# Kernel optimization log

Hardware: AMD Instinct MI355X
Metric: run time of the kernel (lower is better)

## Reference

```python
import jax, jax.numpy as jnp
import numpy as np

NB, DM, DIN, DS, DTR, K = 4, 64, 128, 16, 4, 4
C, COUT, H, W, BATCH, NH = 256, 256, 32, 32, 4, 8


def layernorm(x, w, b, eps=1e-5):
    mu = x.mean(-1, keepdims=True)
    var = ((x - mu) ** 2).mean(-1, keepdims=True)
    return (x - mu) * jax.lax.rsqrt(var + eps) * w + b


def ln_hw(x, eps=1e-5):
    # F.layer_norm(x, [H, W]) -> normalize over last two dims, no affine
    mu = x.mean((-2, -1), keepdims=True)
    var = ((x - mu) ** 2).mean((-2, -1), keepdims=True)
    return (x - mu) * jax.lax.rsqrt(var + eps)


def conv1d(x, w, b, groups=1, pad=1):
    # x: (B, Cin, L), w: (Cout, Cin//groups, k)
    y = jax.lax.conv_general_dilated(x, w, (1,), [(pad, pad)],
                                     dimension_numbers=('NCH', 'OIH', 'NCH'),
                                     feature_group_count=groups)
    return y + b[None, :, None]


def selective_scan(u, dt, Bm, Cm, A, Dp):
    # u, dt: (B,L,din); Bm, Cm: (B,L,ds); A: (din,ds); Dp: (din,)
    dA = jnp.exp(dt[..., None] * A)                     # (B,L,din,ds)
    dBu = (dt * u)[..., None] * Bm[:, :, None, :]       # (B,L,din,ds)

    def step(h, inp):
        dA_t, dBu_t, C_t = inp
        h = dA_t * h + dBu_t
        return h, jnp.einsum('bds,bs->bd', h, C_t)

    h0 = jnp.zeros((u.shape[0], DIN, DS), u.dtype)
    _, ys = jax.lax.scan(step, h0, (dA.transpose(1, 0, 2, 3), dBu.transpose(1, 0, 2, 3), Cm.transpose(1, 0, 2)))
    return ys.transpose(1, 0, 2) + u * Dp


def mamba(xs, inw, convw, convb, xpw, dtw, dtb, alog, dp, outw):
    # xs: (B,L,DM) one branch of Mamba(d_model=DM, d_state=DS, d_conv=K, expand=2)
    xz = xs @ inw.T                                     # (B,L,2*DIN)
    u, z = jnp.split(xz, 2, axis=-1)
    # causal depthwise conv1d (torch pads K-1 and truncates to L == left pad K-1)
    uc = jax.lax.conv_general_dilated(u.transpose(0, 2, 1), convw[:, None, :], (1,), [(K - 1, 0)],
                                      dimension_numbers=('NCH', 'OIH', 'NCH'),
                                      feature_group_count=DIN) + convb[None, :, None]
    u = jax.nn.silu(uc.transpose(0, 2, 1))              # (B,L,DIN)
    xdbc = u @ xpw.T                                    # (B,L,DTR+2*DS)
    dt = jax.nn.softplus(xdbc[..., :DTR] @ dtw.T + dtb)
    Bm, Cm = xdbc[..., DTR:DTR + DS], xdbc[..., DTR + DS:]
    y = selective_scan(u, dt, Bm, Cm, -jnp.exp(alog), dp)
    return (y * jax.nn.silu(z)) @ outw.T


mamba_v = jax.vmap(mamba)  # over branch axis 0 of inputs and all params


def mha(x, inw, inb, outw, outb):
    B, N, Cc = x.shape
    hd = Cc // NH
    qkv = x @ inw.T + inb
    q, k, v = jnp.split(qkv, 3, axis=-1)
    q = q.reshape(B, N, NH, hd).transpose(0, 2, 1, 3)
    k = k.reshape(B, N, NH, hd).transpose(0, 2, 1, 3)
    v = v.reshape(B, N, NH, hd).transpose(0, 2, 1, 3)
    att = jax.nn.softmax((q @ k.transpose(0, 1, 3, 2)) * (1.0 / (hd ** 0.5)), axis=-1)
    o = (att @ v).transpose(0, 2, 1, 3).reshape(B, N, Cc)
    return o @ outw.T + outb


def reference(x, norm_w, norm_b, skip_scale, m_inw, m_convw, m_convb, m_xpw, m_dtw, m_dtb, m_alog, m_d, m_outw, qdw_w, qdw_b, qpw_w, qpw_b, rdw_w, rdw_b, rpw_w, rpw_b, fdw_w, fdw_b, fpw_w, fpw_b, lc_w, lc_b, attn_inw, attn_inb, attn_outw, attn_outb, lgn_w, lgn_b, fc_w, fc_b, dwc_w, dwc_b, proj_w, proj_b):
    B, Cc, Hh, Ww = x.shape
    N = Hh * Ww
    xs = x.reshape(B, Cc, N).transpose(0, 2, 1)         # (B,N,C)
    xn = layernorm(xs, norm_w, norm_b)
    # channel-chunk into NB branches: (NB,B,N,DM)
    xc = xn.reshape(B, N, NB, DM).transpose(2, 0, 1, 3)
    xm = mamba_v(xc, m_inw, m_convw, m_convb, m_xpw, m_dtw, m_dtb, m_alog, m_d, m_outw) + skip_scale * xc
    x_concat = xm.transpose(1, 2, 0, 3).reshape(B, N, Cc)
    # branch gating: depthwise grouped conv (C->NB) then pointwise (NB->NB)
    Q = conv1d(conv1d(x_concat.transpose(0, 2, 1), qdw_w, qdw_b, groups=NB, pad=1), qpw_w, qpw_b, groups=1, pad=0)
    g = jax.nn.sigmoid(Q)                               # (B,NB,N)
    xg = (g.transpose(1, 0, 2)[..., None] * xm).transpose(1, 2, 0, 3).reshape(B, N, Cc)
    xgt = xg.transpose(0, 2, 1)                          # (B,C,N)
    R = conv1d(conv1d(xgt, rdw_w, rdw_b, groups=Cc, pad=1), rpw_w, rpw_b, groups=1, pad=0) + xgt
    cat = jnp.concatenate([xs, R.transpose(0, 2, 1)], axis=-1).transpose(0, 2, 1)  # (B,2C,N)
    xm2 = conv1d(conv1d(cat, fdw_w, fdw_b, groups=2 * Cc, pad=1), fpw_w, fpw_b, groups=1, pad=0) + cat[:, :Cc, :]
    xm2 = xm2.transpose(0, 2, 1)                         # (B,N,C)
    # local-global feature mixing
    x_local = conv1d(xm2.transpose(0, 2, 1), lc_w, lc_b, groups=Cc, pad=1).transpose(0, 2, 1)
    x_global = mha(xm2, attn_inw, attn_inb, attn_outw, attn_outb)
    x_out = jnp.concatenate([x_local, x_global], axis=-1) @ fc_w.T + fc_b
    x_out = jax.nn.gelu(layernorm(x_out, lgn_w, lgn_b), approximate=False)
    # DepthwiseConvolution: layer_norm over [H,W] (no affine) then depthwise conv2d
    xi = x_out.transpose(0, 2, 1).reshape(B, Cc, Hh, Ww)
    xi = ln_hw(xi)
    xi = jax.lax.conv_general_dilated(xi, dwc_w, (1, 1), [(1, 1), (1, 1)],
                                      dimension_numbers=('NCHW', 'OIHW', 'NCHW'),
                                      feature_group_count=Cc) + dwc_b[None, :, None, None]
    x_mixed = xi.reshape(B, Cc, N).transpose(0, 2, 1)
    x_mixed = layernorm(x_mixed, norm_w, norm_b)        # self.norm reused
    x_mixed = x_mixed @ proj_w.T + proj_b
    return x_mixed.transpose(0, 2, 1).reshape(B, COUT, Hh, Ww)


def setup_inputs() -> dict:
    key = jax.random.key(0)
    ks = iter(jax.random.split(key, 64))

    def rn(shape, s=0.02):
        return jax.random.normal(next(ks), shape, jnp.float32) * s

    return dict(
        x=jax.random.normal(next(ks), (BATCH, C, H, W), jnp.float32),
        norm_w=jnp.ones((C,), jnp.float32), norm_b=jnp.zeros((C,), jnp.float32),
        skip_scale=jnp.ones((1,), jnp.float32),
        m_inw=rn((NB, 2 * DIN, DM)), m_convw=rn((NB, DIN, K), 0.2), m_convb=jnp.zeros((NB, DIN), jnp.float32),
        m_xpw=rn((NB, DTR + 2 * DS, DIN)), m_dtw=rn((NB, DIN, DTR), 0.2), m_dtb=rn((NB, DIN), 0.5),
        m_alog=jnp.tile(jnp.log(jnp.arange(1, DS + 1, dtype=jnp.float32)), (NB, DIN, 1)),
        m_d=jnp.ones((NB, DIN), jnp.float32), m_outw=rn((NB, DM, DIN)),
        qdw_w=rn((NB, C // NB, 3), 0.1), qdw_b=jnp.zeros((NB,), jnp.float32),
        qpw_w=rn((NB, NB, 1), 0.3), qpw_b=jnp.zeros((NB,), jnp.float32),
        rdw_w=rn((C, 1, 3), 0.2), rdw_b=jnp.zeros((C,), jnp.float32),
        rpw_w=rn((C, C, 1)), rpw_b=jnp.zeros((C,), jnp.float32),
        fdw_w=rn((2 * C, 1, 3), 0.2), fdw_b=jnp.zeros((2 * C,), jnp.float32),
        fpw_w=rn((C, 2 * C, 1)), fpw_b=jnp.zeros((C,), jnp.float32),
        lc_w=rn((C, 1, 3), 0.2), lc_b=jnp.zeros((C,), jnp.float32),
        attn_inw=rn((3 * C, C)), attn_inb=jnp.zeros((3 * C,), jnp.float32),
        attn_outw=rn((C, C)), attn_outb=jnp.zeros((C,), jnp.float32),
        lgn_w=jnp.ones((C,), jnp.float32), lgn_b=jnp.zeros((C,), jnp.float32),
        fc_w=rn((C, 2 * C)), fc_b=jnp.zeros((C,), jnp.float32),
        dwc_w=rn((C, 1, 3, 3), 0.2), dwc_b=jnp.zeros((C,), jnp.float32),
        proj_w=rn((COUT, C)), proj_b=jnp.zeros((COUT,), jnp.float32),
    )
```

## Files before the change

### kernel.cpp

```cpp
#include <hip/hip_runtime.h>
#include <math.h>


namespace {
constexpr int NB_ = 4, DM_ = 64, DIN_ = 128, DS_ = 16, DTR_ = 4;
constexpr int C_ = 256, N_ = 1024, B_ = 4, HD_ = 32;
constexpr int NCH = 16, LCH = 64;
constexpr int NSTATE = 16 * 128 * 16;
}

typedef __attribute__((ext_vector_type(8))) short bf16x8;
typedef __attribute__((ext_vector_type(4))) float f32x4;
typedef __attribute__((ext_vector_type(8))) unsigned short ushort8v;
typedef __attribute__((ext_vector_type(4))) unsigned short ushort4v;

__device__ __forceinline__ unsigned short f2b(float f) {
  unsigned int u = __float_as_uint(f);
  unsigned int r = u + 0x7FFFu + ((u >> 16) & 1u);
  return (unsigned short)(r >> 16);
}

__device__ __forceinline__ float2 blockReduce2(float a, float b, float* red) {
#pragma unroll
  for (int m = 1; m < 64; m <<= 1) {
    a += __shfl_xor(a, m, 64);
    b += __shfl_xor(b, m, 64);
  }
  int w = threadIdx.x >> 6;
  if ((threadIdx.x & 63) == 0) { red[2 * w] = a; red[2 * w + 1] = b; }
  __syncthreads();
  float ra = red[0] + red[2] + red[4] + red[6];
  float rb = red[1] + red[3] + red[5] + red[7];
  return make_float2(ra, rb);
}

__device__ __forceinline__ float siluf(float x) { return x / (1.f + expf(-x)); }
__device__ __forceinline__ float sigmf(float x) { return 1.f / (1.f + expf(-x)); }
__device__ __forceinline__ float softplusf(float x) {
  return fmaxf(x, 0.f) + log1pf(expf(-fabsf(x)));
}

__global__ __launch_bounds__(256) void k_ln_t2(const float* __restrict__ in,
                                               const float* __restrict__ w,
                                               const float* __restrict__ bias,
                                               float* __restrict__ out_ln) {
  __shared__ float tile[256][17];
  __shared__ float redp[16][16][2];
  __shared__ float stats[16][2];
  int bx = blockIdx.x;
  int b = bx >> 6, n0 = (bx & 63) * 16;
  int c = threadIdx.x;
  {
    const float* p = in + ((long)(b * C_ + c)) * N_ + n0;
#pragma unroll
    for (int j = 0; j < 16; ++j) tile[c][j] = p[j];
  }
  __syncthreads();
  {
    int n = c & 15, g = c >> 4;
    float a = 0.f, q = 0.f;
#pragma unroll
    for (int i = 0; i < 16; ++i) {
      float v = tile[g * 16 + i][n];
      a += v; q += v * v;
    }
    redp[g][n][0] = a; redp[g][n][1] = q;
  }
  __syncthreads();
  if (c < 16) {
    float a = 0.f, q = 0.f;
#pragma unroll
    for (int g2 = 0; g2 < 16; ++g2) { a += redp[g2][c][0]; q += redp[g2][c][1]; }
    float mu = a * (1.f / C_);
    float rs = rsqrtf(q * (1.f / C_) - mu * mu + 1e-5f);
    stats[c][0] = mu; stats[c][1] = rs;
  }
  __syncthreads();
  float wv = w[c], bv = bias[c];
#pragma unroll
  for (int j = 0; j < 16; ++j) {
    float v = tile[c][j];
    long o = ((long)(b * N_ + n0 + j)) * C_ + c;
    out_ln[o] = (v - stats[j][0]) * stats[j][1] * wv + bv;
  }
}

__global__ __launch_bounds__(256) void k_inproj_conv(const float* __restrict__ xn,
                                                     const float* __restrict__ inw,
                                                     const float* __restrict__ cw,
                                                     const float* __restrict__ cb,
                                                     float* __restrict__ U,
                                                     float* __restrict__ Z) {
  __shared__ unsigned short xa[64][72];
  __shared__ unsigned short wb[64][72];
  __shared__ float ut[67][65];
  int r0 = blockIdx.x * 64;
  int nb = blockIdx.y >> 2, q = blockIdx.y & 3, c0 = q * 64;
  int t = threadIdx.x;
  int wv = t >> 6, lane = t & 63, g = lane >> 4, ql = lane & 15;
  const f32x4 zf = {0.f, 0.f, 0.f, 0.f};
  f32x4 acc[4] = {zf, zf, zf, zf};
  int rr = t >> 2, kq = (t & 3) * 16;
  {
    const float* xsrc = xn + (long)(r0 + rr) * C_ + nb * 64 + kq;
#pragma unroll
    for (int j = 0; j < 4; ++j) {
      float4 v = *(const float4*)(xsrc + 4 * j);
      ushort4v u = {f2b(v.x), f2b(v.y), f2b(v.z), f2b(v.w)};
      *(ushort4v*)&xa[rr][kq + 4 * j] = u;
    }
    const float* wsrc = inw + ((long)nb * 256 + c0 + rr) * 64 + kq;
#pragma unroll
    for (int j = 0; j < 4; ++j) {
      float4 v = *(const float4*)(wsrc + 4 * j);
      ushort4v u = {f2b(v.x), f2b(v.y), f2b(v.z), f2b(v.w)};
      *(ushort4v*)&wb[rr][kq + 4 * j] = u;
    }
  }
  __syncthreads();
#pragma unroll
  for (int ks = 0; ks < 2; ++ks) {
    bf16x8 a = *(const bf16x8*)&xa[wv * 16 + ql][ks * 32 + g * 8];
#pragma unroll
    for (int ct = 0; ct < 4; ++ct) {
      bf16x8 b = *(const bf16x8*)&wb[ct * 16 + ql][ks * 32 + g * 8];
      acc[ct] = __builtin_amdgcn_mfma_f32_16x16x32_bf16(a, b, acc[ct], 0, 0, 0);
    }
  }
  if (q < 2) {
#pragma unroll
    for (int ct = 0; ct < 4; ++ct)
#pragma unroll
      for (int reg = 0; reg < 4; ++reg)
        ut[3 + wv * 16 + g * 4 + reg][ct * 16 + ql] = acc[ct][reg];
    if (t < 192) {
      int hr = t >> 6, lc = t & 63;
      float hv = 0.f;
      if ((r0 & 1023) != 0) {
        const float* xrow = xn + (long)(r0 - 3 + hr) * C_ + nb * 64;
        const float* wrow = inw + ((long)nb * 256 + c0 + lc) * 64;
#pragma unroll 8
        for (int k = 0; k < 64; ++k) hv += xrow[k] * wrow[k];
      }
      ut[hr][lc] = hv;
    }
    __syncthreads();
#pragma unroll
    for (int ct = 0; ct < 4; ++ct) {
      int lc = ct * 16 + ql;
      int d = c0 + lc;
      const float* cwp = cw + (nb * DIN_ + d) * 4;
      float w0 = cwp[0], w1 = cwp[1], w2 = cwp[2], w3 = cwp[3];
      float bv = cb[nb * DIN_ + d];
#pragma unroll
      for (int reg = 0; reg < 4; ++reg) {
        int lr = wv * 16 + g * 4 + reg;
        float a = bv + w3 * ut[3 + lr][lc] + w2 * ut[2 + lr][lc] +
                  w1 * ut[1 + lr][lc] + w0 * ut[lr][lc];
        long row = (long)nb * 4096 + r0 + lr;
        U[row * DIN_ + d] = siluf(a);
      }
    }
  } else {
#pragma unroll
    for (int ct = 0; ct < 4; ++ct) {
      int col = c0 - 128 + ct * 16 + ql;
#pragma unroll
      for (int reg = 0; reg < 4; ++reg) {
        long row = (long)nb * 4096 + r0 + wv * 16 + g * 4 + reg;
        Z[row * DIN_ + col] = acc[ct][reg];
      }
    }
  }
}

__global__ __launch_bounds__(256) void k_xdbc_mfma(const float* __restrict__ U,
                                                   const float* __restrict__ xpw,
                                                   const float* __restrict__ dtw,
                                                   const float* __restrict__ dtb,
                                                   float* __restrict__ DT,
                                                   float* __restrict__ BMb,
                                                   float* __restrict__ CMb) {
  __shared__ unsigned short xa[64][72];
  __shared__ unsigned short wb[48][72];
  __shared__ float xd_s[64][40];
  __shared__ float dtw_s[128][4];
  __shared__ float dtb_s[128];
  int t = threadIdx.x;
  long row0 = (long)blockIdx.x * 64;
  int nb = blockIdx.x >> 6;
  for (int i = t; i < 512; i += 256) dtw_s[i >> 2][i & 3] = dtw[nb * 512 + i];
  if (t < 128) dtb_s[t] = dtb[nb * DIN_ + t];
  int wv = t >> 6, lane = t & 63, g = lane >> 4, ql = lane & 15;
  const f32x4 zf = {0.f, 0.f, 0.f, 0.f};
  f32x4 acc[3] = {zf, zf, zf};
  int rr = t >> 2, kq = (t & 3) * 16;
  for (int k0 = 0; k0 < 128; k0 += 64) {
    __syncthreads();
    const float* xsrc = U + (row0 + rr) * DIN_ + k0 + kq;
#pragma unroll
    for (int j = 0; j < 4; ++j) {
      float4 v = *(const float4*)(xsrc + 4 * j);
      ushort4v u = {f2b(v.x), f2b(v.y), f2b(v.z), f2b(v.w)};
      *(ushort4v*)&xa[rr][kq + 4 * j] = u;
    }
    if (rr < 48) {
      if (rr < 36) {
        const float* wsrc = xpw + (long)nb * 36 * 128 + rr * 128 + k0 + kq;
#pragma unroll
        for (int j = 0; j < 4; ++j) {
          float4 v = *(const float4*)(wsrc + 4 * j);
          ushort4v u = {f2b(v.x), f2b(v.y), f2b(v.z), f2b(v.w)};
          *(ushort4v*)&wb[rr][kq + 4 * j] = u;
        }
      } else {
        ushort4v z = {0, 0, 0, 0};
#pragma unroll
        for (int j = 0; j < 4; ++j) *(ushort4v*)&wb[rr][kq + 4 * j] = z;
      }
    }
    __syncthreads();
#pragma unroll
    for (int ks = 0; ks < 2; ++ks) {
      bf16x8 a = *(const bf16x8*)&xa[wv * 16 + ql][ks * 32 + g * 8];
#pragma unroll
      for (int ct = 0; ct < 3; ++ct) {
        bf16x8 b = *(const bf16x8*)&wb[ct * 16 + ql][ks * 32 + g * 8];
        acc[ct] = __builtin_amdgcn_mfma_f32_16x16x32_bf16(a, b, acc[ct], 0, 0, 0);
      }
    }
  }
#pragma unroll
  for (int ct = 0; ct < 3; ++ct) {
    int col = ct * 16 + ql;
    if (col < 36) {
#pragma unroll
      for (int reg = 0; reg < 4; ++reg)
        xd_s[wv * 16 + g * 4 + reg][col] = acc[ct][reg];
    }
  }
  __syncthreads();
  {
    int r = t >> 2, sq = (t & 3) * 4;
    float4 bm4 = make_float4(xd_s[r][4 + sq], xd_s[r][5 + sq],
                             xd_s[r][6 + sq], xd_s[r][7 + sq]);
    *(float4*)&BMb[(row0 + r) * DS_ + sq] = bm4;
    float4 cm4 = make_float4(xd_s[r][20 + sq], xd_s[r][21 + sq],
                             xd_s[r][22 + sq], xd_s[r][23 + sq]);
    *(float4*)&CMb[(row0 + r) * DS_ + sq] = cm4;
  }
  {
    int r = t >> 2, dg = t & 3;
    float x0 = xd_s[r][0], x1 = xd_s[r][1], x2 = xd_s[r][2], x3 = xd_s[r][3];
    float* dst = DT + (row0 + r) * DIN_ + dg * 32;
#pragma unroll
    for (int j = 0; j < 8; ++j) {
      float o[4];
#pragma unroll
      for (int e = 0; e < 4; ++e) {
        int d = dg * 32 + j * 4 + e;
        float a = dtb_s[d] + x0 * dtw_s[d][0] + x1 * dtw_s[d][1] +
                  x2 * dtw_s[d][2] + x3 * dtw_s[d][3];
        o[e] = softplusf(a);
      }
      *(float4*)(dst + j * 4) = make_float4(o[0], o[1], o[2], o[3]);
    }
  }
}

__global__ __launch_bounds__(256) void k_scanA(const float* __restrict__ DT,
                                               const float* __restrict__ U,
                                               const float* __restrict__ BMb,
                                               const float* __restrict__ alog,
                                               float* __restrict__ Aprod,
                                               float* __restrict__ Hend) {
  __shared__ float dt_s[64][64];
  __shared__ float u_s[64][64];
  __shared__ float bm_s[64][16];
  int bx = blockIdx.x;
  int chunk = bx >> 5, rem = bx & 31, nbb = rem >> 1, dh = rem & 1;
  int nb = nbb >> 2;
  int t = threadIdx.x;
  int dl = t >> 2, sg = t & 3;
  int d = dh * 64 + dl;
  long base = (long)nbb * N_ + chunk * LCH;
#pragma unroll
  for (int j = 0; j < 4; ++j) {
    int f = t + 256 * j;
    int tt = f >> 4, dq = (f & 15) * 4;
    long src = (base + tt) * DIN_ + dh * 64 + dq;
    *(float4*)&dt_s[tt][dq] = *(const float4*)&DT[src];
    *(float4*)&u_s[tt][dq]  = *(const float4*)&U[src];
  }
  {
    int tt = t >> 2, sq = (t & 3) * 4;
    *(float4*)&bm_s[tt][sq] = *(const float4*)&BMb[(base + tt) * DS_ + sq];
  }
  float A[4];
#pragma unroll
  for (int i = 0; i < 4; ++i)
    A[i] = -expf(alog[(nb * DIN_ + d) * DS_ + sg * 4 + i]);
  __syncthreads();
  float h[4] = {0.f, 0.f, 0.f, 0.f};
  float ap[4] = {1.f, 1.f, 1.f, 1.f};
  for (int tt = 0; tt < LCH; ++tt) {
    float dtv = dt_s[tt][dl];
    float uv  = u_s[tt][dl];
    float cc = dtv * uv;
    float4 bm4 = *(const float4*)&bm_s[tt][sg * 4];
    float bmv[4] = {bm4.x, bm4.y, bm4.z, bm4.w};
#pragma unroll
    for (int i = 0; i < 4; ++i) {
      float dA = __expf(dtv * A[i]);
      h[i] = dA * h[i] + cc * bmv[i];
      ap[i] *= dA;
    }
  }
  long st = (long)chunk * NSTATE + ((nbb << 7) + d) * 16 + sg * 4;
  *(float4*)&Aprod[st] = make_float4(ap[0], ap[1], ap[2], ap[3]);
  *(float4*)&Hend[st]  = make_float4(h[0], h[1], h[2], h[3]);
}

__global__ __launch_bounds__(256) void k_scanC(float* __restrict__ DT,
                                               const float* __restrict__ U,
                                               const float* __restrict__ BMb,
                                               const float* __restrict__ CMb,
                                               const float* __restrict__ alog,
                                               const float* __restrict__ Dp,
                                               const float* __restrict__ Aprod,
                                               const float* __restrict__ Hend) {
  __shared__ float dt_s[64][64];
  __shared__ float u_s[64][64];
  __shared__ float bm_s[64][16];
  __shared__ float cm_s[64][16];
  int bx = blockIdx.x;
  int chunk = bx >> 5, rem = bx & 31, nbb = rem >> 1, dh = rem & 1;
  int nb = nbb >> 2;
  int t = threadIdx.x;
  int dl = t >> 2, sg = t & 3;
  int d = dh * 64 + dl;
  long base = (long)nbb * N_ + chunk * LCH;
#pragma unroll
  for (int j = 0; j < 4; ++j) {
    int f = t + 256 * j;
    int tt = f >> 4, dq = (f & 15) * 4;
    long src = (base + tt) * DIN_ + dh * 64 + dq;
    *(float4*)&dt_s[tt][dq] = *(const float4*)&DT[src];
    *(float4*)&u_s[tt][dq]  = *(const float4*)&U[src];
  }
  {
    int tt = t >> 2, sq = (t & 3) * 4;
    *(float4*)&bm_s[tt][sq] = *(const float4*)&BMb[(base + tt) * DS_ + sq];
    *(float4*)&cm_s[tt][sq] = *(const float4*)&CMb[(base + tt) * DS_ + sq];
  }
  float A[4];
#pragma unroll
  for (int i = 0; i < 4; ++i)
    A[i] = -expf(alog[(nb * DIN_ + d) * DS_ + sg * 4 + i]);
  float Dv = Dp[nb * DIN_ + d];
  float h[4] = {0.f, 0.f, 0.f, 0.f};
  {
    long state4 = ((nbb << 7) + d) * 16 + sg * 4;
    for (int c = 0; c < chunk; ++c) {
      float4 a4 = *(const float4*)&Aprod[(long)c * NSTATE + state4];
      float4 e4 = *(const float4*)&Hend[(long)c * NSTATE + state4];
      h[0] = e4.x + a4.x * h[0];
      h[1] = e4.y + a4.y * h[1];
      h[2] = e4.z + a4.z * h[2];
      h[3] = e4.w + a4.w * h[3];
    }
  }
  __syncthreads();
  for (int tt = 0; tt < LCH; ++tt) {
    float dtv = dt_s[tt][dl];
    float uv  = u_s[tt][dl];
    float cc = dtv * uv;
    float4 bm4 = *(const float4*)&bm_s[tt][sg * 4];
    float4 cm4 = *(const float4*)&cm_s[tt][sg * 4];
    float bmv[4] = {bm4.x, bm4.y, bm4.z, bm4.w};
    float cmv[4] = {cm4.x, cm4.y, cm4.z, cm4.w};
    float p = 0.f;
#pragma unroll
    for (int i = 0; i < 4; ++i) {
      float dA = __expf(dtv * A[i]);
      h[i] = dA * h[i] + cc * bmv[i];
      p += h[i] * cmv[i];
    }
    p += __shfl_xor(p, 1, 64);
    p += __shfl_xor(p, 2, 64);
    if (sg == 0) DT[(base + tt) * DIN_ + d] = p + Dv * uv;
  }
}

__global__ __launch_bounds__(256) void k_outproj_mfma(const float* __restrict__ Y,
                                                      const float* __restrict__ Zb,
                                                      const float* __restrict__ outw,
                                                      const float* __restrict__ xn,
                                                      const float* __restrict__ skip,
                                                      float* __restrict__ XMC) {
  __shared__ unsigned short xa[64][72];
  __shared__ unsigned short wb[64][72];
  int r0 = blockIdx.x * 64;
  int nb = blockIdx.y;
  int t = threadIdx.x;
  int wv = t >> 6, lane = t & 63, g = lane >> 4, ql = lane & 15;
  const f32x4 zf = {0.f, 0.f, 0.f, 0.f};
  f32x4 acc[4] = {zf, zf, zf, zf};
  int rr = t >> 2, kq = (t & 3) * 16;
  for (int k0 = 0; k0 < 128; k0 += 64) {
    __syncthreads();
    long row = (long)nb * 4096 + r0 + rr;
    const float* ysrc = Y + row * DIN_ + k0 + kq;
    const float* zsrc = Zb + row * DIN_ + k0 + kq;
#pragma unroll
    for (int j = 0; j < 4; ++j) {
      float4 yv = *(const float4*)(ysrc + 4 * j);
      float4 zv = *(const float4*)(zsrc + 4 * j);
      ushort4v u = {f2b(yv.x * siluf(zv.x)), f2b(yv.y * siluf(zv.y)),
                    f2b(yv.z * siluf(zv.z)), f2b(yv.w * siluf(zv.w))};
      *(ushort4v*)&xa[rr][kq + 4 * j] = u;
    }
    const float* wsrc = outw + ((long)nb * 64 + rr) * 128 + k0 + kq;
#pragma unroll
    for (int j = 0; j < 4; ++j) {
      float4 v = *(const float4*)(wsrc + 4 * j);
      ushort4v u = {f2b(v.x), f2b(v.y), f2b(v.z), f2b(v.w)};
      *(ushort4v*)&wb[rr][kq + 4 * j] = u;
    }
    __syncthreads();
#pragma unroll
    for (int ks = 0; ks < 2; ++ks) {
      bf16x8 a = *(const bf16x8*)&xa[wv * 16 + ql][ks * 32 + g * 8];
#pragma unroll
      for (int ct = 0; ct < 4; ++ct) {
        bf16x8 b = *(const bf16x8*)&wb[ct * 16 + ql][ks * 32 + g * 8];
        acc[ct] = __builtin_amdgcn_mfma_f32_16x16x32_bf16(a, b, acc[ct], 0, 0, 0);
      }
    }
  }
  float sk = skip[0];
#pragma unroll
  for (int ct = 0; ct < 4; ++ct) {
    int col = ct * 16 + ql;
#pragma unroll
    for (int reg = 0; reg < 4; ++reg) {
      int bn = r0 + wv * 16 + g * 4 + reg;
      long oc = (long)bn * C_ + nb * 64 + col;
      XMC[oc] = acc[ct][reg] + sk * xn[oc];
    }
  }
}

__global__ __launch_bounds__(256) void k_gate(const float* __restrict__ XMC,
                                              const float* __restrict__ qdw_w,
                                              const float* __restrict__ qdw_b,
                                              const float* __restrict__ qpw_w,
                                              const float* __restrict__ qpw_b,
                                              float* __restrict__ G) {
  int t = threadIdx.x;
  int gid = (blockIdx.x * 256 + t) >> 4;
  int cq = t & 3, p = (t >> 2) & 3;
  int b = gid >> 10, n = gid & 1023;
  float a = 0.f;
#pragma unroll
  for (int k = 0; k < 3; ++k) {
    int nn = n + k - 1;
    if (nn < 0 || nn >= N_) continue;
    const float* xr = XMC + ((long)b * N_ + nn) * C_ + p * 64 + cq * 16;
    const float* wr = qdw_w + (p * 64 + cq * 16) * 3 + k;
#pragma unroll
    for (int i = 0; i < 16; ++i) a += xr[i] * wr[i * 3];
  }
  a += __shfl_xor(a, 1, 64);
  a += __shfl_xor(a, 2, 64);
  float q1 = a + qdw_b[p];
  int lane = t & 63;
  float q1g[4];
#pragma unroll
  for (int pp = 0; pp < 4; ++pp) q1g[pp] = __shfl(q1, (lane & ~12) | (pp << 2), 64);
  int o = p;
  float r = qpw_b[o];
#pragma unroll
  for (int pp = 0; pp < 4; ++pp) r += qpw_w[o * 4 + pp] * q1g[pp];
  if (cq == 0) G[((long)b * 4 + o) * N_ + n] = sigmf(r);
}

__global__ __launch_bounds__(256) void k_xg(const float* __restrict__ XMC,
                                            const float* __restrict__ G,
                                            float* __restrict__ XG) {
  __shared__ float tile[64][65];
  int bx = blockIdx.x;
  int b = bx >> 6, ct = (bx >> 4) & 3, nt = bx & 15;
  int c0 = ct * 64, n0 = nt * 64;
  int t = threadIdx.x;
  {
    int cc = t & 63, nq = t >> 6;
#pragma unroll
    for (int j = 0; j < 16; ++j) {
      int nn = nq * 16 + j;
      tile[cc][nn] = XMC[((long)(b * N_ + n0 + nn)) * C_ + c0 + cc];
    }
  }
  __syncthreads();
  {
    int nl = t & 63, cq = t >> 6;
    float g = G[((long)(b * 4 + ct)) * N_ + n0 + nl];
#pragma unroll
    for (int j = 0; j < 16; ++j) {
      int cl = cq * 16 + j;
      XG[((long)(b * C_ + c0 + cl)) * N_ + n0 + nl] = g * tile[cl][nl];
    }
  }
}

template <int KD>
__global__ __launch_bounds__(256) void k_gemm_cm_dw(const float* __restrict__ inA,
                                                    const float* __restrict__ inB,
                                                    const float* __restrict__ dww,
                                                    const float* __restrict__ dwb,
                                                    const float* __restrict__ w,
                                                    const float* __restrict__ bias,
                                                    const float* __restrict__ residCM,
                                                    const float* __restrict__ residXCM,
                                                    float* __restrict__ outCM,
                                                    float* __restrict__ outRM) {
  __shared__ unsigned short xa[64][72];
  __shared__ unsigned short wb[64][72];
  int rb = blockIdx.x;
  int b = rb >> 4, n0 = (rb & 15) * 64;
  int c0 = blockIdx.y * 64;
  int t = threadIdx.x;
  int wv = t >> 6, lane = t & 63, g = lane >> 4, ql = lane & 15;
  const f32x4 zf = {0.f, 0.f, 0.f, 0.f};
  f32x4 acc[4] = {zf, zf, zf, zf};
  int rr = t >> 2, kq = (t & 3) * 16;
  for (int k0 = 0; k0 < KD; k0 += 64) {
    __syncthreads();
    {
      int k = k0 + rr;
      const float* src = (inB != nullptr && k >= 256)
                             ? inB + ((long)(b * 256 + k - 256)) * 1024
                             : inA + ((long)(b * 256 + k)) * 1024;
      float w0 = dww[k * 3], w1 = dww[k * 3 + 1], w2 = dww[k * 3 + 2], bv = dwb[k];
#pragma unroll
      for (int j = 0; j < 4; ++j) {
        int nb4 = n0 + kq + 4 * j;
        float4 v = *(const float4*)&src[nb4];
        float vm1 = (nb4 > 0) ? src[nb4 - 1] : 0.f;
        float vp4 = (nb4 + 4 < 1024) ? src[nb4 + 4] : 0.f;
        xa[kq + 4 * j + 0][rr] = f2b(bv + w0 * vm1 + w1 * v.x + w2 * v.y);
        xa[kq + 4 * j + 1][rr] = f2b(bv + w0 * v.x + w1 * v.y + w2 * v.z);
        xa[kq + 4 * j + 2][rr] = f2b(bv + w0 * v.y + w1 * v.z + w2 * v.w);
        xa[kq + 4 * j + 3][rr] = f2b(bv + w0 * v.z + w1 * v.w + w2 * vp4);
      }
    }
    const float* wsrc = w + (long)(c0 + rr) * KD + k0 + kq;
#pragma unroll
    for (int j = 0; j < 4; ++j) {
      float4 v = *(const float4*)(wsrc + 4 * j);
      ushort4v u = {f2b(v.x), f2b(v.y), f2b(v.z), f2b(v.w)};
      *(ushort4v*)&wb[rr][kq + 4 * j] = u;
    }
    __syncthreads();
#pragma unroll
    for (int ks = 0; ks < 2; ++ks) {
      bf16x8 a = *(const bf16x8*)&xa[wv * 16 + ql][ks * 32 + g * 8];
#pragma unroll
      for (int ct = 0; ct < 4; ++ct) {
        bf16x8 bfr = *(const bf16x8*)&wb[ct * 16 + ql][ks * 32 + g * 8];
        acc[ct] = __builtin_amdgcn_mfma_f32_16x16x32_bf16(a, bfr, acc[ct], 0, 0, 0);
      }
    }
  }
#pragma unroll
  for (int ct = 0; ct < 4; ++ct) {
    int col = c0 + ct * 16 + ql;
    float bv = bias[col];
    if (outCM) {
      long base = ((long)(b * 256 + col)) * 1024 + n0 + wv * 16 + g * 4;
      float4 r4 = *(const float4*)(residCM + base);
      float4 o = make_float4(acc[ct][0] + bv + r4.x, acc[ct][1] + bv + r4.y,
                             acc[ct][2] + bv + r4.z, acc[ct][3] + bv + r4.w);
      *(float4*)(outCM + base) = o;
    } else {
      int nbase = n0 + wv * 16 + g * 4;
      float4 r4 = *(const float4*)&residXCM[((long)(b * 256 + col)) * 1024 + nbase];
      float rv[4] = {r4.x, r4.y, r4.z, r4.w};
#pragma unroll
      for (int reg = 0; reg < 4; ++reg) {
        long row = (long)b * 1024 + nbase + reg;
        outRM[row * 256 + col] = acc[ct][reg] + bv + rv[reg];
      }
    }
  }
}

template <int KD>
__global__ __launch_bounds__(256) void k_gemm_rm(const float* __restrict__ inA,
                                                 const float* __restrict__ w,
                                                 const float* __restrict__ bias,
                                                 float* __restrict__ out, int Cout) {
  __shared__ unsigned short xa[64][72];
  __shared__ unsigned short wb[64][72];
  int r0 = blockIdx.x * 64;
  int c0 = blockIdx.y * 64;
  int t = threadIdx.x;
  int wv = t >> 6, lane = t & 63, g = lane >> 4, ql = lane & 15;
  const f32x4 zf = {0.f, 0.f, 0.f, 0.f};
  f32x4 acc[4] = {zf, zf, zf, zf};
  int rr = t >> 2, kq = (t & 3) * 16;
  for (int k0 = 0; k0 < KD; k0 += 64) {
    __syncthreads();
    int kk = k0 + kq;
    const float* xsrc = inA + (long)(r0 + rr) * KD + kk;
#pragma unroll
    for (int j = 0; j < 4; ++j) {
      float4 v = *(const float4*)(xsrc + 4 * j);
      ushort4v u = {f2b(v.x), f2b(v.y), f2b(v.z), f2b(v.w)};
      *(ushort4v*)&xa[rr][kq + 4 * j] = u;
    }
    const float* wsrc = w + (long)(c0 + rr) * KD + kk;
#pragma unroll
    for (int j = 0; j < 4; ++j) {
      float4 v = *(const float4*)(wsrc + 4 * j);
      ushort4v u = {f2b(v.x), f2b(v.y), f2b(v.z), f2b(v.w)};
      *(ushort4v*)&wb[rr][kq + 4 * j] = u;
    }
    __syncthreads();
#pragma unroll
    for (int ks = 0; ks < 2; ++ks) {
      bf16x8 a = *(const bf16x8*)&xa[wv * 16 + ql][ks * 32 + g * 8];
#pragma unroll
      for (int ct = 0; ct < 4; ++ct) {
        bf16x8 b = *(const bf16x8*)&wb[ct * 16 + ql][ks * 32 + g * 8];
        acc[ct] = __builtin_amdgcn_mfma_f32_16x16x32_bf16(a, b, acc[ct], 0, 0, 0);
      }
    }
  }
#pragma unroll
  for (int ct = 0; ct < 4; ++ct) {
    int col = c0 + ct * 16 + ql;
    float bv = bias[col];
#pragma unroll
    for (int reg = 0; reg < 4; ++reg) {
      long row = r0 + wv * 16 + g * 4 + reg;
      out[row * Cout + col] = acc[ct][reg] + bv;
    }
  }
}

__global__ __launch_bounds__(256) void k_gemm_qkv(const float* __restrict__ in,
                                                  const float* __restrict__ w,
                                                  const float* __restrict__ bias,
                                                  unsigned short* __restrict__ out) {
  __shared__ unsigned short xa[64][72];
  __shared__ unsigned short wb[64][72];
  int r0 = blockIdx.x * 64;
  int c0 = blockIdx.y * 64;
  int t = threadIdx.x;
  int wv = t >> 6, lane = t & 63, g = lane >> 4, ql = lane & 15;
  const f32x4 zf = {0.f, 0.f, 0.f, 0.f};
  f32x4 acc[4] = {zf, zf, zf, zf};
  int rr = t >> 2, kq = (t & 3) * 16;
  for (int k0 = 0; k0 < 256; k0 += 64) {
    __syncthreads();
    const float* xsrc = in + (long)(r0 + rr) * 256 + k0 + kq;
#pragma unroll
    for (int j = 0; j < 4; ++j) {
      float4 v = *(const float4*)(xsrc + 4 * j);
      ushort4v u = {f2b(v.x), f2b(v.y), f2b(v.z), f2b(v.w)};
      *(ushort4v*)&xa[rr][kq + 4 * j] = u;
    }
    const float* wsrc = w + (long)(c0 + rr) * 256 + k0 + kq;
#pragma unroll
    for (int j = 0; j < 4; ++j) {
      float4 v = *(const float4*)(wsrc + 4 * j);
      ushort4v u = {f2b(v.x), f2b(v.y), f2b(v.z), f2b(v.w)};
      *(ushort4v*)&wb[rr][kq + 4 * j] = u;
    }
    __syncthreads();
#pragma unroll
    for (int ks = 0; ks < 2; ++ks) {
      bf16x8 a = *(const bf16x8*)&xa[wv * 16 + ql][ks * 32 + g * 8];
#pragma unroll
      for (int ct = 0; ct < 4; ++ct) {
        bf16x8 b = *(const bf16x8*)&wb[ct * 16 + ql][ks * 32 + g * 8];
        acc[ct] = __builtin_amdgcn_mfma_f32_16x16x32_bf16(a, b, acc[ct], 0, 0, 0);
      }
    }
  }
#pragma unroll
  for (int ct = 0; ct < 4; ++ct) {
    int col = c0 + ct * 16 + ql;
    float bv = bias[col];
#pragma unroll
    for (int reg = 0; reg < 4; ++reg) {
      long row = r0 + wv * 16 + g * 4 + reg;
      out[row * 768 + col] = f2b(acc[ct][reg] + bv);
    }
  }
}

__global__ __launch_bounds__(256) void k_gemm_fc(const float* __restrict__ XM2,
                                                 const float* __restrict__ XGL,
                                                 const float* __restrict__ lcw,
                                                 const float* __restrict__ lcb,
                                                 const float* __restrict__ w,
                                                 const float* __restrict__ bias,
                                                 float* __restrict__ out) {
  __shared__ unsigned short xa[64][72];
  __shared__ unsigned short wb[64][72];
  int r0 = blockIdx.x * 64;
  int c0 = blockIdx.y * 64;
  int t = threadIdx.x;
  int wv = t >> 6, lane = t & 63, g = lane >> 4, ql = lane & 15;
  const f32x4 zf = {0.f, 0.f, 0.f, 0.f};
  f32x4 acc[4] = {zf, zf, zf, zf};
  int rr = t >> 2, kq = (t & 3) * 16;
  for (int k0 = 0; k0 < 512; k0 += 64) {
    __syncthreads();
    int kk = k0 + kq;
    long row = r0 + rr;
    if (kk < 256) {
      int n = (int)(row & 1023);
      const float* pc = XM2 + row * 256 + kk;
      bool hm = n > 0, hp = n < 1023;
#pragma unroll
      for (int j = 0; j < 4; ++j) {
        float4 v = *(const float4*)(pc + 4 * j);
        float4 vm = hm ? *(const float4*)(pc - 256 + 4 * j) : make_float4(0.f, 0.f, 0.f, 0.f);
        float4 vp = hp ? *(const float4*)(pc + 256 + 4 * j) : make_float4(0.f, 0.f, 0.f, 0.f);
        int c = kk + 4 * j;
        xa[rr][kq + 4 * j + 0] = f2b(lcb[c + 0] + lcw[(c + 0) * 3] * vm.x + lcw[(c + 0) * 3 + 1] * v.x + lcw[(c + 0) * 3 + 2] * vp.x);
        xa[rr][kq + 4 * j + 1] = f2b(lcb[c + 1] + lcw[(c + 1) * 3] * vm.y + lcw[(c + 1) * 3 + 1] * v.y + lcw[(c + 1) * 3 + 2] * vp.y);
        xa[rr][kq + 4 * j + 2] = f2b(lcb[c + 2] + lcw[(c + 2) * 3] * vm.z + lcw[(c + 2) * 3 + 1] * v.z + lcw[(c + 2) * 3 + 2] * vp.z);
        xa[rr][kq + 4 * j + 3] = f2b(lcb[c + 3] + lcw[(c + 3) * 3] * vm.w + lcw[(c + 3) * 3 + 1] * v.w + lcw[(c + 3) * 3 + 2] * vp.w);
      }
    } else {
      const float* xsrc = XGL + row * 256 + (kk - 256);
#pragma unroll
      for (int j = 0; j < 4; ++j) {
        float4 v = *(const float4*)(xsrc + 4 * j);
        ushort4v u = {f2b(v.x), f2b(v.y), f2b(v.z), f2b(v.w)};
        *(ushort4v*)&xa[rr][kq + 4 * j] = u;
      }
    }
    const float* wsrc = w + (long)(c0 + rr) * 512 + kk;
#pragma unroll
    for (int j = 0; j < 4; ++j) {
      float4 v = *(const float4*)(wsrc + 4 * j);
      ushort4v u = {f2b(v.x), f2b(v.y), f2b(v.z), f2b(v.w)};
      *(ushort4v*)&wb[rr][kq + 4 * j] = u;
    }
    __syncthreads();
#pragma unroll
    for (int ks = 0; ks < 2; ++ks) {
      bf16x8 a = *(const bf16x8*)&xa[wv * 16 + ql][ks * 32 + g * 8];
#pragma unroll
      for (int ct = 0; ct < 4; ++ct) {
        bf16x8 b = *(const bf16x8*)&wb[ct * 16 + ql][ks * 32 + g * 8];
        acc[ct] = __builtin_amdgcn_mfma_f32_16x16x32_bf16(a, b, acc[ct], 0, 0, 0);
      }
    }
  }
#pragma unroll
  for (int ct = 0; ct < 4; ++ct) {
    int col = c0 + ct * 16 + ql;
    float bv = bias[col];
#pragma unroll
    for (int reg = 0; reg < 4; ++reg) {
      long row = r0 + wv * 16 + g * 4 + reg;
      out[row * 256 + col] = acc[ct][reg] + bv;
    }
  }
}

__global__ __launch_bounds__(256) void k_attn_mfma(const unsigned short* __restrict__ qkvb,
                                                   float* __restrict__ O) {
  __shared__ unsigned short K_lds[64 * 40];
  __shared__ unsigned short Vt_lds[32 * 72];
  __shared__ unsigned short P_lds[4][16 * 72];
  int bx = blockIdx.x;
  int bh = bx >> 4, qt = bx & 15;
  int b = bh >> 3, h = bh & 7;
  int t = threadIdx.x;
  int w = t >> 6, lane = t & 63;
  int g = lane >> 4, ql = lane & 15;
  const float qscale = 0.17677669529663687f * 1.44269504088896341f;

  bf16x8 q_frag = *(const bf16x8*)(qkvb + ((long)(b * N_ + qt * 64 + w * 16 + ql)) * 768 + h * HD_ + g * 8);
  float m = -1e30f, l = 0.f;
  f32x4 o_acc[2];
  const f32x4 zf = {0.f, 0.f, 0.f, 0.f};
  o_acc[0] = zf; o_acc[1] = zf;

  for (int kt = 0; kt < 16; ++kt) {
    __syncthreads();
    {
      int kr = t >> 2, d0 = (t & 3) * 8;
      const unsigned short* gp = qkvb + ((long)(b * N_ + kt * 64 + kr)) * 768 + 256 + h * HD_ + d0;
      ushort8v kv = *(const ushort8v*)gp;
      *(ushort8v*)&K_lds[kr * 40 + d0] = kv;
      ushort8v vv = *(const ushort8v*)(gp + 256);
#pragma unroll
      for (int i = 0; i < 8; ++i) Vt_lds[(d0 + i) * 72 + kr] = vv[i];
    }
    __syncthreads();
    f32x4 s_frag[4];
#pragma unroll
    for (int s = 0; s < 4; ++s) {
      bf16x8 k_frag = *(const bf16x8*)&K_lds[(s * 16 + ql) * 40 + g * 8];
      s_frag[s] = __builtin_amdgcn_mfma_f32_16x16x32_bf16(k_frag, q_frag, zf, 0, 0, 0);
    }
    float sv[16];
#pragma unroll
    for (int s = 0; s < 4; ++s)
#pragma unroll
      for (int r = 0; r < 4; ++r) sv[s * 4 + r] = s_frag[s][r] * qscale;
    float tmax = sv[0];
#pragma unroll
    for (int i = 1; i < 16; ++i) tmax = fmaxf(tmax, sv[i]);
    tmax = fmaxf(tmax, __shfl_xor(tmax, 16));
    tmax = fmaxf(tmax, __shfl_xor(tmax, 32));
    float mn = fmaxf(m, tmax);
    float corr = exp2f(m - mn);
    float psum = 0.f;
    unsigned short pb[16];
#pragma unroll
    for (int i = 0; i < 16; ++i) {
      float p = exp2f(sv[i] - mn);
      psum += p;
      pb[i] = f2b(p);
    }
    psum += __shfl_xor(psum, 16);
    psum += __shfl_xor(psum, 32);
    l = l * corr + psum;
    m = mn;
#pragma unroll
    for (int mt = 0; mt < 2; ++mt)
#pragma unroll
      for (int r = 0; r < 4; ++r) o_acc[mt][r] *= corr;
#pragma unroll
    for (int s = 0; s < 4; ++s) {
      ushort4v p4 = {pb[s * 4], pb[s * 4 + 1], pb[s * 4 + 2], pb[s * 4 + 3]};
      *(ushort4v*)&P_lds[w][ql * 72 + s * 16 + g * 4] = p4;
    }
#pragma unroll
    for (int c = 0; c < 2; ++c) {
      bf16x8 p_frag = *(const bf16x8*)&P_lds[w][ql * 72 + c * 32 + g * 8];
#pragma unroll
      for (int mt = 0; mt < 2; ++mt) {
        bf16x8 v_frag = *(const bf16x8*)&Vt_lds[(mt * 16 + ql) * 72 + c * 32 + g * 8];
        o_acc[mt] = __builtin_amdgcn_mfma_f32_16x16x32_bf16(v_frag, p_frag, o_acc[mt], 0, 0, 0);
      }
    }
  }
  float inv = 1.f / l;
  float* op = O + ((long)(b * N_ + qt * 64 + w * 16 + ql)) * C_ + h * HD_;
#pragma unroll
  for (int mt = 0; mt < 2; ++mt) {
    float4 o4 = make_float4(o_acc[mt][0] * inv, o_acc[mt][1] * inv,
                            o_acc[mt][2] * inv, o_acc[mt][3] * inv);
    *(float4*)(op + mt * 16 + g * 4) = o4;
  }
}

__global__ __launch_bounds__(256) void k_lngelu(const float* __restrict__ XO,
                                                const float* __restrict__ lw,
                                                const float* __restrict__ lb,
                                                float* __restrict__ XI) {
  __shared__ float tile[256][17];
  __shared__ float redp[16][16][2];
  __shared__ float stats[16][2];
  int bx = blockIdx.x;
  int b = bx >> 6, n0 = (bx & 63) * 16;
  int c = threadIdx.x;
#pragma unroll
  for (int j = 0; j < 16; ++j)
    tile[c][j] = XO[((long)(b * N_ + n0 + j)) * C_ + c];
  __syncthreads();
  {
    int n = c & 15, g = c >> 4;
    float a = 0.f, q = 0.f;
#pragma unroll
    for (int i = 0; i < 16; ++i) {
      float v = tile[g * 16 + i][n];
      a += v; q += v * v;
    }
    redp[g][n][0] = a; redp[g][n][1] = q;
  }
  __syncthreads();
  if (c < 16) {
    float a = 0.f, q = 0.f;
#pragma unroll
    for (int g2 = 0; g2 < 16; ++g2) { a += redp[g2][c][0]; q += redp[g2][c][1]; }
    float mu = a * (1.f / C_);
    float rs = rsqrtf(q * (1.f / C_) - mu * mu + 1e-5f);
    stats[c][0] = mu; stats[c][1] = rs;
  }
  __syncthreads();
  float wv = lw[c], bv = lb[c];
  float o[16];
#pragma unroll
  for (int j = 0; j < 16; ++j) {
    float x = (tile[c][j] - stats[j][0]) * stats[j][1] * wv + bv;
    o[j] = 0.5f * x * (1.f + erff(x * 0.70710678118654752f));
  }
  float* dst = &XI[((long)(b * C_ + c)) * N_ + n0];
#pragma unroll
  for (int j4 = 0; j4 < 4; ++j4)
    *(float4*)(dst + j4 * 4) = make_float4(o[4 * j4], o[4 * j4 + 1], o[4 * j4 + 2], o[4 * j4 + 3]);
}

__global__ __launch_bounds__(256) void k_lnhw_dwc(const float* __restrict__ XIin,
                                                  const float* __restrict__ w,
                                                  const float* __restrict__ bias,
                                                  float* __restrict__ XD) {
  __shared__ float pl[32][33];
  __shared__ float red[8];
  long base = (long)blockIdx.x * 1024;
  int c = blockIdx.x & 255;
  int t = threadIdx.x;
  float4 v = *(const float4*)&XIin[base + t * 4];
  float a = v.x + v.y + v.z + v.w;
  float q = v.x * v.x + v.y * v.y + v.z * v.z + v.w * v.w;
  float2 s = blockReduce2(a, q, red);
  float mu = s.x * (1.f / 1024.f);
  float rs = rsqrtf(s.y * (1.f / 1024.f) - mu * mu + 1e-5f);
  int hh = t >> 3, w0 = (t & 7) * 4;
  pl[hh][w0 + 0] = (v.x - mu) * rs;
  pl[hh][w0 + 1] = (v.y - mu) * rs;
  pl[hh][w0 + 2] = (v.z - mu) * rs;
  pl[hh][w0 + 3] = (v.w - mu) * rs;
  __syncthreads();
  float wk[9];
#pragma unroll
  for (int i = 0; i < 9; ++i) wk[i] = w[c * 9 + i];
  float bv = bias[c];
  float o[4];
#pragma unroll
  for (int j = 0; j < 4; ++j) {
    int ww = w0 + j;
    float acc = bv;
#pragma unroll
    for (int kh = 0; kh < 3; ++kh) {
      int h2 = hh + kh - 1;
      if (h2 < 0 || h2 >= 32) continue;
#pragma unroll
      for (int kw = 0; kw < 3; ++kw) {
        int w2 = ww + kw - 1;
        if (w2 < 0 || w2 >= 32) continue;
        acc += wk[kh * 3 + kw] * pl[h2][w2];
      }
    }
    o[j] = acc;
  }
  *(float4*)&XD[base + t * 4] = make_float4(o[0], o[1], o[2], o[3]);
}

__global__ __launch_bounds__(256) void k_lnproj(const float* __restrict__ XD,
                                                const float* __restrict__ nw,
                                                const float* __restrict__ nbias,
                                                const float* __restrict__ w,
                                                const float* __restrict__ bias,
                                                float* __restrict__ out) {
  __shared__ unsigned short xa[64][72];
  __shared__ unsigned short wb[64][72];
  __shared__ float ps[4][64], pq[4][64];
  __shared__ float mu_s[64], rs_s[64];
  int rb = blockIdx.x;
  int b = rb >> 4, n0 = (rb & 15) * 64;
  int c0 = blockIdx.y * 64;
  int t = threadIdx.x;
  {
    int nl = t & 63, cq = t >> 6;
    const float* src = XD + ((long)(b * 256 + cq * 64)) * 1024 + n0 + nl;
    float s = 0.f, q = 0.f;
    for (int i = 0; i < 64; ++i) {
      float v = src[(long)i * 1024];
      s += v; q += v * v;
    }
    ps[cq][nl] = s; pq[cq][nl] = q;
  }
  __syncthreads();
  if (t < 64) {
    float s = ps[0][t] + ps[1][t] + ps[2][t] + ps[3][t];
    float q = pq[0][t] + pq[1][t] + pq[2][t] + pq[3][t];
    float mu = s * (1.f / 256.f);
    float rs = rsqrtf(q * (1.f / 256.f) - mu * mu + 1e-5f);
    mu_s[t] = mu; rs_s[t] = rs;
  }
  int wv = t >> 6, lane = t & 63, g = lane >> 4, ql = lane & 15;
  const f32x4 zf = {0.f, 0.f, 0.f, 0.f};
  f32x4 acc[4] = {zf, zf, zf, zf};
  int rr = t >> 2, kq = (t & 3) * 16;
  for (int k0 = 0; k0 < 256; k0 += 64) {
    __syncthreads();
    {
      int ch = k0 + rr;
      const float* src = XD + ((long)(b * 256 + ch)) * 1024 + n0 + kq;
      float wv_ = nw[ch], bv_ = nbias[ch];
#pragma unroll
      for (int j = 0; j < 4; ++j) {
        float4 v = *(const float4*)(src + 4 * j);
        int n = kq + 4 * j;
        xa[n + 0][rr] = f2b((v.x - mu_s[n + 0]) * rs_s[n + 0] * wv_ + bv_);
        xa[n + 1][rr] = f2b((v.y - mu_s[n + 1]) * rs_s[n + 1] * wv_ + bv_);
        xa[n + 2][rr] = f2b((v.z - mu_s[n + 2]) * rs_s[n + 2] * wv_ + bv_);
        xa[n + 3][rr] = f2b((v.w - mu_s[n + 3]) * rs_s[n + 3] * wv_ + bv_);
      }
      const float* wsrc = w + (long)(c0 + rr) * 256 + k0 + kq;
#pragma unroll
      for (int j = 0; j < 4; ++j) {
        float4 v = *(const float4*)(wsrc + 4 * j);
        ushort4v u = {f2b(v.x), f2b(v.y), f2b(v.z), f2b(v.w)};
        *(ushort4v*)&wb[rr][kq + 4 * j] = u;
      }
    }
    __syncthreads();
#pragma unroll
    for (int ks = 0; ks < 2; ++ks) {
      bf16x8 a = *(const bf16x8*)&xa[wv * 16 + ql][ks * 32 + g * 8];
#pragma unroll
      for (int ct = 0; ct < 4; ++ct) {
        bf16x8 bfr = *(const bf16x8*)&wb[ct * 16 + ql][ks * 32 + g * 8];
        acc[ct] = __builtin_amdgcn_mfma_f32_16x16x32_bf16(a, bfr, acc[ct], 0, 0, 0);
      }
    }
  }
#pragma unroll
  for (int ct = 0; ct < 4; ++ct) {
    int col = c0 + ct * 16 + ql;
    float bv = bias[col];
    long basei = ((long)(b * 256 + col)) * 1024 + n0 + wv * 16 + g * 4;
    *(float4*)(out + basei) = make_float4(acc[ct][0] + bv, acc[ct][1] + bv,
                                          acc[ct][2] + bv, acc[ct][3] + bv);
  }
}

extern "C" void kernel_launch(void* const* d_in, const int* in_sizes, int n_in,
                              void* d_out, int out_size, void* d_ws, size_t ws_size,
                              hipStream_t stream) {
  const float* x        = (const float*)d_in[0];
  const float* norm_w   = (const float*)d_in[1];
  const float* norm_b   = (const float*)d_in[2];
  const float* skip     = (const float*)d_in[3];
  const float* m_inw    = (const float*)d_in[4];
  const float* m_convw  = (const float*)d_in[5];
  const float* m_convb  = (const float*)d_in[6];
  const float* m_xpw    = (const float*)d_in[7];
  const float* m_dtw    = (const float*)d_in[8];
  const float* m_dtb    = (const float*)d_in[9];
  const float* m_alog   = (const float*)d_in[10];
  const float* m_d      = (const float*)d_in[11];
  const float* m_outw   = (const float*)d_in[12];
  const float* qdw_w    = (const float*)d_in[13];
  const float* qdw_b    = (const float*)d_in[14];
  const float* qpw_w    = (const float*)d_in[15];
  const float* qpw_b    = (const float*)d_in[16];
  const float* rdw_w    = (const float*)d_in[17];
  const float* rdw_b    = (const float*)d_in[18];
  const float* rpw_w    = (const float*)d_in[19];
  const float* rpw_b    = (const float*)d_in[20];
  const float* fdw_w    = (const float*)d_in[21];
  const float* fdw_b    = (const float*)d_in[22];
  const float* fpw_w    = (const float*)d_in[23];
  const float* fpw_b    = (const float*)d_in[24];
  const float* lc_w     = (const float*)d_in[25];
  const float* lc_b     = (const float*)d_in[26];
  const float* attn_inw = (const float*)d_in[27];
  const float* attn_inb = (const float*)d_in[28];
  const float* attn_outw= (const float*)d_in[29];
  const float* attn_outb= (const float*)d_in[30];
  const float* lgn_w    = (const float*)d_in[31];
  const float* lgn_b    = (const float*)d_in[32];
  const float* fc_w     = (const float*)d_in[33];
  const float* fc_b     = (const float*)d_in[34];
  const float* dwc_w    = (const float*)d_in[35];
  const float* dwc_b    = (const float*)d_in[36];
  const float* proj_w   = (const float*)d_in[37];
  const float* proj_b   = (const float*)d_in[38];
  float* out = (float*)d_out;

  float* ws = (float*)d_ws;
  const size_t F = 1048576;
  float* XN  = ws + 1 * F;
  float* U   = ws + 2 * F;
  float* Z   = ws + 4 * F;
  float* DT  = ws + 6 * F;
  float* BM  = ws + 8 * F;
  float* CM  = ws + 8 * F + F / 4;
  float* XMC = ws + 8 * F + F / 2;
  float* SC_APROD = ws + 8 * F + F / 2;
  float* SC_HEND  = ws + 9 * F;
  float* G   = ws + 0 * F;
  float* XG  = ws + 2 * F;
  float* RB  = ws + 4 * F;
  float* XM2 = ws + 5 * F;
  unsigned short* QKVB = (unsigned short*)(ws + 1 * F);
  float* O   = ws + 4 * F;
  float* XGL = ws + 6 * F;
  float* XO  = ws + 7 * F;
  float* XI  = ws + 8 * F;
  float* XD  = ws + 0 * F;
  (void)ws_size; (void)in_sizes; (void)n_in; (void)out_size;

  k_ln_t2<<<256, 256, 0, stream>>>(x, norm_w, norm_b, XN);
  k_inproj_conv<<<dim3(64, 16), 256, 0, stream>>>(XN, m_inw, m_convw, m_convb, U, Z);
  k_xdbc_mfma<<<256, 256, 0, stream>>>(U, m_xpw, m_dtw, m_dtb, DT, BM, CM);
  k_scanA<<<512, 256, 0, stream>>>(DT, U, BM, m_alog, SC_APROD, SC_HEND);
  k_scanC<<<512, 256, 0, stream>>>(DT, U, BM, CM, m_alog, m_d, SC_APROD, SC_HEND);
  k_outproj_mfma<<<dim3(64, 4), 256, 0, stream>>>(DT, Z, m_outw, XN, skip, XMC);
  k_gate<<<256, 256, 0, stream>>>(XMC, qdw_w, qdw_b, qpw_w, qpw_b, G);
  k_xg<<<256, 256, 0, stream>>>(XMC, G, XG);
  k_gemm_cm_dw<256><<<dim3(64, 4), 256, 0, stream>>>(XG, nullptr, rdw_w, rdw_b,
                                                     rpw_w, rpw_b, XG, nullptr, RB, nullptr);
  k_gemm_cm_dw<512><<<dim3(64, 4), 256, 0, stream>>>(x, RB, fdw_w, fdw_b,
                                                     fpw_w, fpw_b, nullptr, x, nullptr, XM2);
  k_gemm_qkv<<<dim3(64, 12), 256, 0, stream>>>(XM2, attn_inw, attn_inb, QKVB);
  k_attn_mfma<<<512, 256, 0, stream>>>(QKVB, O);
  k_gemm_rm<256><<<dim3(64, 4), 256, 0, stream>>>(O, attn_outw, attn_outb, XGL, 256);
  k_gemm_fc<<<dim3(64, 4), 256, 0, stream>>>(XM2, XGL, lc_w, lc_b, fc_w, fc_b, XO);
  k_lngelu<<<256, 256, 0, stream>>>(XO, lgn_w, lgn_b, XI);
  k_lnhw_dwc<<<1024, 256, 0, stream>>>(XI, dwc_w, dwc_b, XD);
  k_lnproj<<<dim3(64, 4), 256, 0, stream>>>(XD, norm_w, norm_b, proj_w, proj_b, out);
}
```

Measured before the change: 206.3 us.

## Fuse x_proj/dt projection with chunk scan pass A; vectorize gate loads

Merges the xdbc projection kernel with the first chunked-scan pass so that U, DT and B for each 64-row chunk stay in shared memory, avoiding a global round-trip and one launch. Each block now runs the scan serially over both halves of DIN, so it has half as many blocks as the old scanA with twice the sequential work per thread, plus more LDS per block. The gate kernel also loads its 16 input values with float4 vector loads instead of scalar loads.

```diff
diff --git a/kernel.cpp b/kernel.cpp
--- a/kernel.cpp
+++ b/kernel.cpp
@@ -174,21 +174,28 @@
   }
 }
 
-__global__ __launch_bounds__(256) void k_xdbc_mfma(const float* __restrict__ U,
-                                                   const float* __restrict__ xpw,
-                                                   const float* __restrict__ dtw,
-                                                   const float* __restrict__ dtb,
-                                                   float* __restrict__ DT,
-                                                   float* __restrict__ BMb,
-                                                   float* __restrict__ CMb) {
+__global__ __launch_bounds__(256) void k_xdbc_scanA(const float* __restrict__ U,
+                                                    const float* __restrict__ xpw,
+                                                    const float* __restrict__ dtw,
+                                                    const float* __restrict__ dtb,
+                                                    const float* __restrict__ alog,
+                                                    float* __restrict__ DT,
+                                                    float* __restrict__ BMb,
+                                                    float* __restrict__ CMb,
+                                                    float* __restrict__ Aprod,
+                                                    float* __restrict__ Hend) {
   __shared__ unsigned short xa[64][72];
   __shared__ unsigned short wb[48][72];
   __shared__ float xd_s[64][40];
   __shared__ float dtw_s[128][4];
   __shared__ float dtb_s[128];
+  __shared__ float dt_s[64][132];
+  __shared__ float u_s[64][132];
+  __shared__ float bm_s[64][20];
   int t = threadIdx.x;
   long row0 = (long)blockIdx.x * 64;
   int nb = blockIdx.x >> 6;
+  int nbb = blockIdx.x >> 4, chunk = blockIdx.x & 15;
   for (int i = t; i < 512; i += 256) dtw_s[i >> 2][i & 3] = dtw[nb * 512 + i];
   if (t < 128) dtb_s[t] = dtb[nb * DIN_ + t];
   int wv = t >> 6, lane = t & 63, g = lane >> 4, ql = lane & 15;
@@ -201,6 +208,7 @@
 #pragma unroll
     for (int j = 0; j < 4; ++j) {
       float4 v = *(const float4*)(xsrc + 4 * j);
+      *(float4*)&u_s[rr][k0 + kq + 4 * j] = v;
       ushort4v u = {f2b(v.x), f2b(v.y), f2b(v.z), f2b(v.w)};
       *(ushort4v*)&xa[rr][kq + 4 * j] = u;
     }
@@ -245,6 +253,7 @@
     float4 bm4 = make_float4(xd_s[r][4 + sq], xd_s[r][5 + sq],
                              xd_s[r][6 + sq], xd_s[r][7 + sq]);
     *(float4*)&BMb[(row0 + r) * DS_ + sq] = bm4;
+    *(float4*)&bm_s[r][sq] = bm4;
     float4 cm4 = make_float4(xd_s[r][20 + sq], xd_s[r][21 + sq],
                              xd_s[r][22 + sq], xd_s[r][23 + sq]);
     *(float4*)&CMb[(row0 + r) * DS_ + sq] = cm4;
@@ -263,62 +272,41 @@
                   x2 * dtw_s[d][2] + x3 * dtw_s[d][3];
         o[e] = softplusf(a);
       }
-      *(float4*)(dst + j * 4) = make_float4(o[0], o[1], o[2], o[3]);
-    }
-  }
-}
-
-__global__ __launch_bounds__(256) void k_scanA(const float* __restrict__ DT,
-                                               const float* __restrict__ U,
-                                               const float* __restrict__ BMb,
-                                               const float* __restrict__ alog,
-                                               float* __restrict__ Aprod,
-                                               float* __restrict__ Hend) {
-  __shared__ float dt_s[64][64];
-  __shared__ float u_s[64][64];
-  __shared__ float bm_s[64][16];
-  int bx = blockIdx.x;
-  int chunk = bx >> 5, rem = bx & 31, nbb = rem >> 1, dh = rem & 1;
-  int nb = nbb >> 2;
-  int t = threadIdx.x;
-  int dl = t >> 2, sg = t & 3;
-  int d = dh * 64 + dl;
-  long base = (long)nbb * N_ + chunk * LCH;
-#pragma unroll
-  for (int j = 0; j < 4; ++j) {
-    int f = t + 256 * j;
-    int tt = f >> 4, dq = (f & 15) * 4;
-    long src = (base + tt) * DIN_ + dh * 64 + dq;
-    *(float4*)&dt_s[tt][dq] = *(const float4*)&DT[src];
-    *(float4*)&u_s[tt][dq]  = *(const float4*)&U[src];
-  }
+      float4 o4 = make_float4(o[0], o[1], o[2], o[3]);
+      *(float4*)(dst + j * 4) = o4;
+      *(float4*)&dt_s[r][dg * 32 + j * 4] = o4;
+    }
+  }
+  __syncthreads();
   {
-    int tt = t >> 2, sq = (t & 3) * 4;
-    *(float4*)&bm_s[tt][sq] = *(const float4*)&BMb[(base + tt) * DS_ + sq];
-  }
-  float A[4];
-#pragma unroll
-  for (int i = 0; i < 4; ++i)
-    A[i] = -expf(alog[(nb * DIN_ + d) * DS_ + sg * 4 + i]);
-  __syncthreads();
-  float h[4] = {0.f, 0.f, 0.f, 0.f};
-  float ap[4] = {1.f, 1.f, 1.f, 1.f};
-  for (int tt = 0; tt < LCH; ++tt) {
-    float dtv = dt_s[tt][dl];
-    float uv  = u_s[tt][dl];
-    float cc = dtv * uv;
-    float4 bm4 = *(const float4*)&bm_s[tt][sg * 4];
-    float bmv[4] = {bm4.x, bm4.y, bm4.z, bm4.w};
-#pragma unroll
-    for (int i = 0; i < 4; ++i) {
-      float dA = __expf(dtv * A[i]);
-      h[i] = dA * h[i] + cc * bmv[i];
-      ap[i] *= dA;
-    }
-  }
-  long st = (long)chunk * NSTATE + ((nbb << 7) + d) * 16 + sg * 4;
-  *(float4*)&Aprod[st] = make_float4(ap[0], ap[1], ap[2], ap[3]);
-  *(float4*)&Hend[st]  = make_float4(h[0], h[1], h[2], h[3]);
+    int dl = t >> 2, sg = t & 3;
+#pragma unroll
+    for (int dh = 0; dh < 2; ++dh) {
+      int d = dh * 64 + dl;
+      float A[4];
+#pragma unroll
+      for (int i = 0; i < 4; ++i)
+        A[i] = -expf(alog[(nb * DIN_ + d) * DS_ + sg * 4 + i]);
+      float h[4] = {0.f, 0.f, 0.f, 0.f};
+      float ap[4] = {1.f, 1.f, 1.f, 1.f};
+      for (int tt = 0; tt < LCH; ++tt) {
+        float dtv = dt_s[tt][d];
+        float uv  = u_s[tt][d];
+        float cc = dtv * uv;
+        float4 bm4 = *(const float4*)&bm_s[tt][sg * 4];
+        float bmv[4] = {bm4.x, bm4.y, bm4.z, bm4.w};
+#pragma unroll
+        for (int i = 0; i < 4; ++i) {
+          float dA = __expf(dtv * A[i]);
+          h[i] = dA * h[i] + cc * bmv[i];
+          ap[i] *= dA;
+        }
+      }
+      long st = (long)chunk * NSTATE + ((nbb << 7) + d) * 16 + sg * 4;
+      *(float4*)&Aprod[st] = make_float4(ap[0], ap[1], ap[2], ap[3]);
+      *(float4*)&Hend[st]  = make_float4(h[0], h[1], h[2], h[3]);
+    }
+  }
 }
 
 __global__ __launch_bounds__(256) void k_scanC(float* __restrict__ DT,
@@ -468,8 +456,13 @@
     if (nn < 0 || nn >= N_) continue;
     const float* xr = XMC + ((long)b * N_ + nn) * C_ + p * 64 + cq * 16;
     const float* wr = qdw_w + (p * 64 + cq * 16) * 3 + k;
-#pragma unroll
-    for (int i = 0; i < 16; ++i) a += xr[i] * wr[i * 3];
+    float xv[16];
+    *(float4*)&xv[0]  = *(const float4*)(xr);
+    *(float4*)&xv[4]  = *(const float4*)(xr + 4);
+    *(float4*)&xv[8]  = *(const float4*)(xr + 8);
+    *(float4*)&xv[12] = *(const float4*)(xr + 12);
+#pragma unroll
+    for (int i = 0; i < 16; ++i) a += xv[i] * wr[i * 3];
   }
   a += __shfl_xor(a, 1, 64);
   a += __shfl_xor(a, 2, 64);
@@ -1107,8 +1100,8 @@
 
   k_ln_t2<<<256, 256, 0, stream>>>(x, norm_w, norm_b, XN);
   k_inproj_conv<<<dim3(64, 16), 256, 0, stream>>>(XN, m_inw, m_convw, m_convb, U, Z);
-  k_xdbc_mfma<<<256, 256, 0, stream>>>(U, m_xpw, m_dtw, m_dtb, DT, BM, CM);
-  k_scanA<<<512, 256, 0, stream>>>(DT, U, BM, m_alog, SC_APROD, SC_HEND);
+  k_xdbc_scanA<<<256, 256, 0, stream>>>(U, m_xpw, m_dtw, m_dtb, m_alog,
+                                        DT, BM, CM, SC_APROD, SC_HEND);
   k_scanC<<<512, 256, 0, stream>>>(DT, U, BM, CM, m_alog, m_d, SC_APROD, SC_HEND);
   k_outproj_mfma<<<dim3(64, 4), 256, 0, stream>>>(DT, Z, m_outw, XN, skip, XMC);
   k_gate<<<256, 256, 0, stream>>>(XMC, qdw_w, qdw_b, qpw_w, qpw_b, G);
```

Result: no change. 207.1 us (+0.4%).
